# Performance work log

Measured on AMD Instinct MI355X. Metric: run time of the kernel, lower is better.

## Reference

```python
import jax, jax.numpy as jnp
import numpy as np

B, S, E, H, EDGE = 2, 2048, 512, 8, 16
D = E // H  # head_dim = 64


def setup_inputs() -> dict:
    key = jax.random.key(0)
    ks = jax.random.split(key, 10)
    s = 0.02
    return {
        "q": jax.random.normal(ks[0], (B, S, E), dtype=jnp.float32),
        "k": jax.random.normal(ks[1], (B, S, E), dtype=jnp.float32),
        "v": jax.random.normal(ks[2], (B, S, E), dtype=jnp.float32),
        "p": jax.random.normal(ks[3], (B, S, S, EDGE), dtype=jnp.float32),
        "in_proj_w": jax.random.normal(ks[4], (3 * E, E), dtype=jnp.float32) * s,
        "in_proj_b": jnp.zeros((3 * E,), dtype=jnp.float32),
        "out_proj_w": jax.random.normal(ks[5], (E, E), dtype=jnp.float32) * s,
        "out_proj_b": jnp.zeros((E,), dtype=jnp.float32),
        "edge_w": jax.random.normal(ks[6], (H, EDGE), dtype=jnp.float32) * s,
        "edge_b": jnp.zeros((H,), dtype=jnp.float32),
    }


def reference(q, k, v, p, in_proj_w, in_proj_b, out_proj_w, out_proj_b, edge_w, edge_b):
    b, s, e = q.shape
    # edge features -> per-head additive bias: [b,sq,sk,edge] -> [b,h,sq,sk]
    bias = jnp.einsum("bqke,he->bhqk", p, edge_w) + edge_b[None, :, None, None]

    # packed qkv projections (torch Linear: y = x W^T + b)
    wq, wk, wv = jnp.split(in_proj_w, 3, axis=0)
    bq, bk, bv = jnp.split(in_proj_b, 3, axis=0)
    qh = (q @ wq.T + bq).reshape(b, s, H, D).transpose(0, 2, 1, 3)  # bhqd
    kh = (k @ wk.T + bk).reshape(b, s, H, D).transpose(0, 2, 1, 3)  # bhkd
    vh = (v @ wv.T + bv).reshape(b, s, H, D).transpose(0, 2, 1, 3)  # bhkd

    scale = 1.0 / jnp.sqrt(jnp.float32(D))
    scores = jnp.einsum("bhqd,bhkd->bhqk", qh, kh) * scale + bias
    attn = jax.nn.softmax(scores, axis=-1)
    ctx = jnp.einsum("bhqk,bhkd->bhqd", attn, vh)  # [b,h,s,d]
    ctx = ctx.transpose(0, 2, 1, 3).reshape(b, s, e)
    return ctx @ out_proj_w.T + out_proj_b
```

## Files before the change

### kernel.cpp

```cpp
#include <hip/hip_runtime.h>

#define NB 2
#define NS 2048
#define NE 512
#define NH 8
#define ND 64
#define NEDGE 16

typedef unsigned short u16;
typedef __attribute__((ext_vector_type(4))) float f32x4;
typedef __attribute__((ext_vector_type(8))) short bf16x8;

__device__ __forceinline__ u16 f2bf(float f) {
  unsigned u = __float_as_uint(f);
  u += 0x7FFFu + ((u >> 16) & 1u);
  return (u16)(u >> 16);
}
__device__ __forceinline__ void gload16(const void* g, void* l) {
  __builtin_amdgcn_global_load_lds(
      (const __attribute__((address_space(1))) unsigned*)g,
      (__attribute__((address_space(3))) unsigned*)l, 16, 0, 0);
}

__global__ void k_cvt(const float* __restrict__ in, u16* __restrict__ out, int n4) {
  int i = blockIdx.x * 256 + threadIdx.x;
  if (i >= n4) return;
  float4 v = ((const float4*)in)[i];
  ushort4 o;
  o.x = f2bf(v.x); o.y = f2bf(v.y); o.z = f2bf(v.z); o.w = f2bf(v.w);
  ((ushort4*)out)[i] = o;
}

__device__ __forceinline__ void gemm128_core(const u16* __restrict__ A,
                                             const u16* __restrict__ W,
                                             u16* As, u16* Bs,
                                             int mt, f32x4 acc[4][4]) {
  const int tid = threadIdx.x, wave = tid >> 6, lane = tid & 63;
  const int g = lane >> 4, c = lane & 15;
  const int wm = wave >> 1, wn = wave & 1;
  for (int kt = 0; kt < 16; ++kt) {
#pragma unroll
    for (int r = 0; r < 2; ++r) {
      int seg = wave + 4 * r;
      int idx = seg * 64 + lane;
      int row = idx >> 2, colB = idx & 3;
      gload16(A + (size_t)(mt * 128 + row) * 512 + kt * 32 + colB * 8,
              (char*)As + seg * 1024);
      gload16(W + (size_t)row * 512 + kt * 32 + colB * 8,
              (char*)Bs + seg * 1024);
    }
    __syncthreads();
    bf16x8 af[4], bw[4];
#pragma unroll
    for (int mb = 0; mb < 4; ++mb)
      af[mb] = *(const bf16x8*)&As[(wm * 64 + mb * 16 + c) * 32 + 8 * g];
#pragma unroll
    for (int nb = 0; nb < 4; ++nb)
      bw[nb] = *(const bf16x8*)&Bs[(wn * 64 + nb * 16 + c) * 32 + 8 * g];
#pragma unroll
    for (int mb = 0; mb < 4; ++mb)
#pragma unroll
      for (int nb = 0; nb < 4; ++nb)
        acc[mb][nb] = __builtin_amdgcn_mfma_f32_16x16x32_bf16(
            af[mb], bw[nb], acc[mb][nb], 0, 0, 0);
    __syncthreads();
  }
}

__launch_bounds__(256)
__global__ void k_proj(const u16* __restrict__ qbf, const u16* __restrict__ kbf,
                       const u16* __restrict__ vbf, const u16* __restrict__ wbf,
                       const float* __restrict__ bin,
                       u16* __restrict__ qh, u16* __restrict__ kh,
                       u16* __restrict__ vt) {
  __shared__ __align__(16) u16 As[4096];
  __shared__ __align__(16) u16 Bs[4096];
  const int tid = threadIdx.x, wave = tid >> 6, lane = tid & 63;
  const int g = lane >> 4, c = lane & 15;
  const int wm = wave >> 1, wn = wave & 1;
  const int mt = blockIdx.x;
  const int chunk = blockIdx.y >> 2, ntl = blockIdx.y & 3;
  const u16* A = chunk == 0 ? qbf : (chunk == 1 ? kbf : vbf);
  const u16* W = wbf + (size_t)(chunk * 512 + ntl * 128) * 512;

  f32x4 acc[4][4];
#pragma unroll
  for (int i = 0; i < 4; ++i)
#pragma unroll
    for (int j = 0; j < 4; ++j) acc[i][j] = (f32x4){0.f, 0.f, 0.f, 0.f};

  gemm128_core(A, W, As, Bs, mt, acc);

#pragma unroll
  for (int mb = 0; mb < 4; ++mb) {
#pragma unroll
    for (int nb = 0; nb < 4; ++nb) {
      int ncl = ntl * 128 + wn * 64 + nb * 16 + c;
      float bv = bin[chunk * 512 + ncl];
      int h = ncl >> 6, d = ncl & 63;
      int m0 = mt * 128 + wm * 64 + mb * 16 + g * 4;
      int b = m0 >> 11, s0 = m0 & 2047;
      if (chunk == 2) {
        ushort4 o;
        o.x = f2bf(acc[mb][nb][0] + bv);
        o.y = f2bf(acc[mb][nb][1] + bv);
        o.z = f2bf(acc[mb][nb][2] + bv);
        o.w = f2bf(acc[mb][nb][3] + bv);
        *(ushort4*)&vt[((size_t)(b * 8 + h) * 64 + d) * 2048 + s0] = o;
      } else {
        u16* dst = (chunk == 0) ? qh : kh;
        float sc = (chunk == 0) ? 0.125f : 1.0f;
#pragma unroll
        for (int r = 0; r < 4; ++r)
          dst[((size_t)(b * 8 + h) * 2048 + s0 + r) * 64 + d] =
              f2bf((acc[mb][nb][r] + bv) * sc);
      }
    }
  }
}

__device__ __forceinline__ float redmax16(float x) {
  x = fmaxf(x, __shfl_xor(x, 1));
  x = fmaxf(x, __shfl_xor(x, 2));
  x = fmaxf(x, __shfl_xor(x, 4));
  x = fmaxf(x, __shfl_xor(x, 8));
  return x;
}
__device__ __forceinline__ float redsum16(float x) {
  x += __shfl_xor(x, 1); x += __shfl_xor(x, 2);
  x += __shfl_xor(x, 4); x += __shfl_xor(x, 8);
  return x;
}

__launch_bounds__(512, 2)
__global__ void k_fattn(const float* __restrict__ p,
                        const float* __restrict__ ewg, const float* __restrict__ ebg,
                        const u16* __restrict__ qh, const u16* __restrict__ kh,
                        const u16* __restrict__ vt, u16* __restrict__ ctx) {
  __shared__ __align__(16) float p_s[2][16384];
  __shared__ __align__(16) u16 P_s[8][1024];
  const int tid = threadIdx.x;
  const int wave = tid >> 6, lane = tid & 63;
  const int g = lane >> 4, c = lane & 15;
  const int h = wave;
  const int bid = blockIdx.x;
  const int xcd = bid & 7, idx = bid >> 3;
  const int b = xcd >> 2;
  const int qt = (xcd & 3) * 32 + idx;
  const int q0 = qt * 16;
  const int bh = b * 8 + h;
  const int sl = (c >> 1) & 3;
  u16* Pw = P_s[wave];

  float ewh[16];
#pragma unroll
  for (int e = 0; e < 16; ++e) ewh[e] = ewg[h * 16 + e];
  const float ebh = ebg[h];

  const u16* Qb = qh + ((size_t)bh * 2048 + q0 + c) * 64;
  bf16x8 qf0 = *(const bf16x8*)(Qb + 8 * g);
  bf16x8 qf1 = *(const bf16x8*)(Qb + 32 + 8 * g);
  const u16* Kb = kh + (size_t)bh * 2048 * 64;
  const u16* Vb = vt + (size_t)bh * 64 * 2048;

  const float* pb = p + (size_t)(b * 2048 + q0) * 2048 * 16;
  int soff[8], doff[8];
#pragma unroll
  for (int i = 0; i < 8; ++i) {
    int u = i * 512 + tid;
    int ecp = u & 3, kk = (u >> 2) & 63, qq = u >> 8;
    int ecl = ecp ^ ((kk >> 1) & 3);
    soff[i] = (qq * 2048 + kk) * 16 + ecl * 4;
    doff[i] = u * 16;
  }

  f32x4 o[4];
#pragma unroll
  for (int i = 0; i < 4; ++i) o[i] = (f32x4){0.f, 0.f, 0.f, 0.f};
  float mrow[4] = {-1e30f, -1e30f, -1e30f, -1e30f};
  float lrow[4] = {0.f, 0.f, 0.f, 0.f};

#pragma unroll
  for (int i = 0; i < 8; ++i)
    gload16(pb + soff[i], (char*)p_s + doff[i]);

  for (int t = 0; t < 32; ++t) {
    const int kt = t * 64;
    asm volatile("s_waitcnt vmcnt(0)" ::: "memory");
    __builtin_amdgcn_s_barrier();
    __builtin_amdgcn_sched_barrier(0);
    if (t < 31) {
      const float* src = pb + (size_t)(kt + 64) * 16;
      char* dst = (char*)p_s + ((t + 1) & 1) * 65536;
#pragma unroll
      for (int i = 0; i < 8; ++i)
        gload16(src + soff[i], dst + doff[i]);
    }
    __builtin_amdgcn_sched_barrier(0);
    const float* pc = p_s[t & 1];

    float bv[4][4];
#pragma unroll
    for (int nb = 0; nb < 4; ++nb) {
#pragma unroll
      for (int r = 0; r < 4; ++r) {
        const float* ps = pc + (g * 4 + r) * 1024 + (nb * 16 + c) * 16;
        f32x4 a0 = *(const f32x4*)(ps + (0 ^ sl) * 4);
        f32x4 a1 = *(const f32x4*)(ps + (1 ^ sl) * 4);
        f32x4 a2 = *(const f32x4*)(ps + (2 ^ sl) * 4);
        f32x4 a3 = *(const f32x4*)(ps + (3 ^ sl) * 4);
        float d = ebh;
        d += a0[0]*ewh[0] + a0[1]*ewh[1] + a0[2]*ewh[2] + a0[3]*ewh[3];
        d += a1[0]*ewh[4] + a1[1]*ewh[5] + a1[2]*ewh[6] + a1[3]*ewh[7];
        d += a2[0]*ewh[8] + a2[1]*ewh[9] + a2[2]*ewh[10] + a2[3]*ewh[11];
        d += a3[0]*ewh[12] + a3[1]*ewh[13] + a3[2]*ewh[14] + a3[3]*ewh[15];
        bv[nb][r] = d;
      }
    }

    f32x4 sc[4];
#pragma unroll
    for (int nb = 0; nb < 4; ++nb) {
      const u16* kp = Kb + (size_t)(kt + nb * 16 + c) * 64 + 8 * g;
      bf16x8 b0 = *(const bf16x8*)kp;
      bf16x8 b1 = *(const bf16x8*)(kp + 32);
      f32x4 z = (f32x4){0.f, 0.f, 0.f, 0.f};
      z = __builtin_amdgcn_mfma_f32_16x16x32_bf16(qf0, b0, z, 0, 0, 0);
      z = __builtin_amdgcn_mfma_f32_16x16x32_bf16(qf1, b1, z, 0, 0, 0);
      sc[nb] = z;
    }
#pragma unroll
    for (int nb = 0; nb < 4; ++nb)
#pragma unroll
      for (int r = 0; r < 4; ++r) sc[nb][r] += bv[nb][r];

    float mnew[4], scl[4];
#pragma unroll
    for (int r = 0; r < 4; ++r) {
      float mx = fmaxf(fmaxf(sc[0][r], sc[1][r]), fmaxf(sc[2][r], sc[3][r]));
      mx = redmax16(mx);
      mnew[r] = fmaxf(mrow[r], mx);
      scl[r] = __expf(mrow[r] - mnew[r]);
      mrow[r] = mnew[r];
    }
    float rsum[4] = {0.f, 0.f, 0.f, 0.f};
#pragma unroll
    for (int nb = 0; nb < 4; ++nb)
#pragma unroll
      for (int r = 0; r < 4; ++r) {
        float e = __expf(sc[nb][r] - mnew[r]);
        sc[nb][r] = e;
        rsum[r] += e;
      }
#pragma unroll
    for (int r = 0; r < 4; ++r) {
      float s = redsum16(rsum[r]);
      lrow[r] = lrow[r] * scl[r] + s;
    }
#pragma unroll
    for (int nd = 0; nd < 4; ++nd)
#pragma unroll
      for (int r = 0; r < 4; ++r) o[nd][r] *= scl[r];

#pragma unroll
    for (int nb = 0; nb < 4; ++nb)
#pragma unroll
      for (int r = 0; r < 4; ++r) {
        int rr = g * 4 + r, kk = nb * 16 + c;
        Pw[rr * 64 + (kk ^ ((rr & 7) << 3))] = f2bf(sc[nb][r]);
      }
    bf16x8 pa0, pa1;
    {
      int rr = c;
      pa0 = *(const bf16x8*)&Pw[rr * 64 + ((8 * g) ^ ((rr & 7) << 3))];
      pa1 = *(const bf16x8*)&Pw[rr * 64 + ((32 + 8 * g) ^ ((rr & 7) << 3))];
    }
#pragma unroll
    for (int nd = 0; nd < 4; ++nd) {
      const u16* vp = Vb + (size_t)(nd * 16 + c) * 2048 + kt;
      bf16x8 v0 = *(const bf16x8*)(vp + 8 * g);
      bf16x8 v1 = *(const bf16x8*)(vp + 32 + 8 * g);
      o[nd] = __builtin_amdgcn_mfma_f32_16x16x32_bf16(pa0, v0, o[nd], 0, 0, 0);
      o[nd] = __builtin_amdgcn_mfma_f32_16x16x32_bf16(pa1, v1, o[nd], 0, 0, 0);
    }
  }

  float inv[4];
#pragma unroll
  for (int r = 0; r < 4; ++r) inv[r] = 1.0f / lrow[r];
#pragma unroll
  for (int nd = 0; nd < 4; ++nd)
#pragma unroll
    for (int r = 0; r < 4; ++r) {
      int s_glob = q0 + g * 4 + r;
      ctx[(size_t)(b * 2048 + s_glob) * 512 + h * 64 + nd * 16 + c] =
          f2bf(o[nd][r] * inv[r]);
    }
}

__launch_bounds__(256)
__global__ void k_outproj(const u16* __restrict__ ctx, const u16* __restrict__ wobf,
                          const float* __restrict__ bout, float* __restrict__ out) {
  __shared__ __align__(16) u16 As[4096];
  __shared__ __align__(16) u16 Bs[4096];
  const int tid = threadIdx.x, wave = tid >> 6, lane = tid & 63;
  const int g = lane >> 4, c = lane & 15;
  const int wm = wave >> 1, wn = wave & 1;
  const int mt = blockIdx.x, nt = blockIdx.y;
  const u16* W = wobf + (size_t)(nt * 128) * 512;

  f32x4 acc[4][4];
#pragma unroll
  for (int i = 0; i < 4; ++i)
#pragma unroll
    for (int j = 0; j < 4; ++j) acc[i][j] = (f32x4){0.f, 0.f, 0.f, 0.f};

  gemm128_core(ctx, W, As, Bs, mt, acc);

#pragma unroll
  for (int mb = 0; mb < 4; ++mb)
#pragma unroll
    for (int nb = 0; nb < 4; ++nb) {
      int n = nt * 128 + wn * 64 + nb * 16 + c;
      float bv = bout[n];
      int m0 = mt * 128 + wm * 64 + mb * 16 + g * 4;
#pragma unroll
      for (int r = 0; r < 4; ++r)
        out[(size_t)(m0 + r) * 512 + n] = acc[mb][nb][r] + bv;
    }
}

extern "C" void kernel_launch(void* const* d_in, const int* in_sizes, int n_in,
                              void* d_out, int out_size, void* d_ws, size_t ws_size,
                              hipStream_t stream) {
  (void)in_sizes; (void)n_in; (void)out_size; (void)ws_size;
  const float* q     = (const float*)d_in[0];
  const float* k     = (const float*)d_in[1];
  const float* v     = (const float*)d_in[2];
  const float* p     = (const float*)d_in[3];
  const float* w_in  = (const float*)d_in[4];
  const float* b_in  = (const float*)d_in[5];
  const float* w_out = (const float*)d_in[6];
  const float* b_out = (const float*)d_in[7];
  const float* ew    = (const float*)d_in[8];
  const float* eb    = (const float*)d_in[9];
  float* out = (float*)d_out;

  char* ws = (char*)d_ws;
  size_t off = 0;
  auto alloc = [&](size_t bytes) {
    void* r = ws + off;
    off += (bytes + 255) & ~(size_t)255;
    return r;
  };
  const size_t NTOK = (size_t)NB * NS;
  u16* qbf  = (u16*)alloc(NTOK * NE * 2);
  u16* kbf  = (u16*)alloc(NTOK * NE * 2);
  u16* vbf  = (u16*)alloc(NTOK * NE * 2);
  u16* wbf  = (u16*)alloc((size_t)3 * NE * NE * 2);
  u16* wobf = (u16*)alloc((size_t)NE * NE * 2);
  u16* qhb  = (u16*)alloc(NTOK * NE * 2);
  u16* khb  = (u16*)alloc(NTOK * NE * 2);
  u16* vtb  = (u16*)alloc(NTOK * NE * 2);
  u16* ctxb = (u16*)alloc(NTOK * NE * 2);

  int n4;
  n4 = (int)(NTOK * NE / 4);
  k_cvt<<<n4 / 256, 256, 0, stream>>>(q, qbf, n4);
  k_cvt<<<n4 / 256, 256, 0, stream>>>(k, kbf, n4);
  k_cvt<<<n4 / 256, 256, 0, stream>>>(v, vbf, n4);
  n4 = 3 * NE * NE / 4;
  k_cvt<<<n4 / 256, 256, 0, stream>>>(w_in, wbf, n4);
  n4 = NE * NE / 4;
  k_cvt<<<n4 / 256, 256, 0, stream>>>(w_out, wobf, n4);

  k_proj<<<dim3(32, 12), 256, 0, stream>>>(qbf, kbf, vbf, wbf, b_in, qhb, khb, vtb);

  k_fattn<<<256, 512, 0, stream>>>(p, ew, eb, qhb, khb, vtb, ctxb);

  k_outproj<<<dim3(32, 4), 256, 0, stream>>>(ctxb, wobf, b_out, out);
}
```

Before: 894.1 us.

## Compute edge bias with MFMA and share across heads via LDS

Replaces the per-wave scalar FMA edge-bias computation, where each head's wave redundantly read all 16 edge features per (q,k) pair, with a cooperative bf16 MFMA. The MFMA computes all 8 heads' biases for the tile at once and writes them to a shared LDS buffer, and each head's wave then reads its own bias back. P tile loads also switch to a non-temporal cache policy. This cuts LDS reads and VALU work but adds bf16 rounding of p and the bias, plus two extra block barriers per tile.

```diff
diff --git a/kernel.cpp b/kernel.cpp
--- a/kernel.cpp
+++ b/kernel.cpp
@@ -16,10 +16,18 @@
   u += 0x7FFFu + ((u >> 16) & 1u);
   return (u16)(u >> 16);
 }
+__device__ __forceinline__ float bf2f(u16 h) {
+  return __uint_as_float(((unsigned)h) << 16);
+}
 __device__ __forceinline__ void gload16(const void* g, void* l) {
   __builtin_amdgcn_global_load_lds(
       (const __attribute__((address_space(1))) unsigned*)g,
       (__attribute__((address_space(3))) unsigned*)l, 16, 0, 0);
+}
+__device__ __forceinline__ void gload16nt(const void* g, void* l) {
+  __builtin_amdgcn_global_load_lds(
+      (const __attribute__((address_space(1))) unsigned*)g,
+      (__attribute__((address_space(3))) unsigned*)l, 16, 0, 2);
 }
 
 __global__ void k_cvt(const float* __restrict__ in, u16* __restrict__ out, int n4) {
@@ -138,7 +146,7 @@
                         const u16* __restrict__ qh, const u16* __restrict__ kh,
                         const u16* __restrict__ vt, u16* __restrict__ ctx) {
   __shared__ __align__(16) float p_s[2][16384];
-  __shared__ __align__(16) u16 P_s[8][1024];
+  __shared__ __align__(16) u16 aux[8192];
   const int tid = threadIdx.x;
   const int wave = tid >> 6, lane = tid & 63;
   const int g = lane >> 4, c = lane & 15;
@@ -149,13 +157,16 @@
   const int qt = (xcd & 3) * 32 + idx;
   const int q0 = qt * 16;
   const int bh = b * 8 + h;
-  const int sl = (c >> 1) & 3;
-  u16* Pw = P_s[wave];
-
-  float ewh[16];
-#pragma unroll
-  for (int e = 0; e < 16; ++e) ewh[e] = ewg[h * 16 + e];
-  const float ebh = ebg[h];
+  u16* Pw = aux + wave * 1024;
+
+  bf16x8 ewf;
+#pragma unroll
+  for (int i = 0; i < 8; ++i) {
+    int e = g * 8 + i;
+    float val = (c < 8 && e < 16) ? ewg[c * 16 + e] : 0.f;
+    ewf[i] = (short)f2bf(val);
+  }
+  const float ebv = (c < 8) ? ebg[c] : 0.f;
 
   const u16* Qb = qh + ((size_t)bh * 2048 + q0 + c) * 64;
   bf16x8 qf0 = *(const bf16x8*)(Qb + 8 * g);
@@ -182,7 +193,7 @@
 
 #pragma unroll
   for (int i = 0; i < 8; ++i)
-    gload16(pb + soff[i], (char*)p_s + doff[i]);
+    gload16nt(pb + soff[i], (char*)p_s + doff[i]);
 
   for (int t = 0; t < 32; ++t) {
     const int kt = t * 64;
@@ -194,29 +205,57 @@
       char* dst = (char*)p_s + ((t + 1) & 1) * 65536;
 #pragma unroll
       for (int i = 0; i < 8; ++i)
-        gload16(src + soff[i], dst + doff[i]);
+        gload16nt(src + soff[i], dst + doff[i]);
     }
     __builtin_amdgcn_sched_barrier(0);
     const float* pc = p_s[t & 1];
 
+#pragma unroll
+    for (int m = 0; m < 8; ++m) {
+      bf16x8 af;
+      if (g < 2) {
+        int pairl = wave * 128 + m * 16 + c;
+        int qloc = pairl >> 6;
+        int kk = pairl & 63;
+        int swz = (kk >> 1) & 3;
+        const float* ps = pc + (qloc * 256 + kk * 4) * 4;
+        f32x4 a0 = *(const f32x4*)(ps + ((2 * g) ^ swz) * 4);
+        f32x4 a1 = *(const f32x4*)(ps + ((2 * g + 1) ^ swz) * 4);
+        af[0] = (short)f2bf(a0[0]); af[1] = (short)f2bf(a0[1]);
+        af[2] = (short)f2bf(a0[2]); af[3] = (short)f2bf(a0[3]);
+        af[4] = (short)f2bf(a1[0]); af[5] = (short)f2bf(a1[1]);
+        af[6] = (short)f2bf(a1[2]); af[7] = (short)f2bf(a1[3]);
+      } else {
+        af = (bf16x8){0, 0, 0, 0, 0, 0, 0, 0};
+      }
+      f32x4 cz = (f32x4){0.f, 0.f, 0.f, 0.f};
+      f32x4 bc = __builtin_amdgcn_mfma_f32_16x16x32_bf16(af, ewf, cz, 0, 0, 0);
+      if (c < 8) {
+#pragma unroll
+        for (int i = 0; i < 4; ++i) {
+          int pairl = wave * 128 + m * 16 + g * 4 + i;
+          int qloc = pairl >> 6, kk = pairl & 63;
+          int kp = kk ^ ((qloc >> 2) << 2);
+          aux[(qloc * 64 + kp) * 8 + c] = f2bf(bc[i] + ebv);
+        }
+      }
+    }
+    asm volatile("s_waitcnt lgkmcnt(0)" ::: "memory");
+    __builtin_amdgcn_s_barrier();
+    __builtin_amdgcn_sched_barrier(0);
+
     float bv[4][4];
 #pragma unroll
-    for (int nb = 0; nb < 4; ++nb) {
+    for (int nb = 0; nb < 4; ++nb)
 #pragma unroll
       for (int r = 0; r < 4; ++r) {
-        const float* ps = pc + (g * 4 + r) * 1024 + (nb * 16 + c) * 16;
-        f32x4 a0 = *(const f32x4*)(ps + (0 ^ sl) * 4);
-        f32x4 a1 = *(const f32x4*)(ps + (1 ^ sl) * 4);
-        f32x4 a2 = *(const f32x4*)(ps + (2 ^ sl) * 4);
-        f32x4 a3 = *(const f32x4*)(ps + (3 ^ sl) * 4);
-        float d = ebh;
-        d += a0[0]*ewh[0] + a0[1]*ewh[1] + a0[2]*ewh[2] + a0[3]*ewh[3];
-        d += a1[0]*ewh[4] + a1[1]*ewh[5] + a1[2]*ewh[6] + a1[3]*ewh[7];
-        d += a2[0]*ewh[8] + a2[1]*ewh[9] + a2[2]*ewh[10] + a2[3]*ewh[11];
-        d += a3[0]*ewh[12] + a3[1]*ewh[13] + a3[2]*ewh[14] + a3[3]*ewh[15];
-        bv[nb][r] = d;
-      }
-    }
+        int qloc = g * 4 + r;
+        int kp = (nb * 16 + c) ^ (g << 2);
+        bv[nb][r] = bf2f(aux[(qloc * 64 + kp) * 8 + h]);
+      }
+    asm volatile("s_waitcnt lgkmcnt(0)" ::: "memory");
+    __builtin_amdgcn_s_barrier();
+    __builtin_amdgcn_sched_barrier(0);
 
     f32x4 sc[4];
 #pragma unroll
```

New measurement: 870.4 us. 1.03x faster.
